# Performance work log

Hardware: AMD Instinct MI355X
Metric: run time of the kernel (lower is better)

The kernel has to match this reference:

```python
import jax, jax.numpy as jnp
import numpy as np
import math

D = 512; H = 8; DH = D // H; DFF = 4 * D
B = 128; S = 100; N_LAYERS = 6; VOCAB = 300 + 3
SCALE = 1.0 / math.sqrt(DH)


def _sinusoid(positions, d):
    # standard sinusoidal encoding, valid for negative (relative) positions too
    div = jnp.exp(jnp.arange(0, d, 2, dtype=jnp.float32) * (-math.log(10000.0) / d))
    ang = positions[:, None].astype(jnp.float32) * div[None, :]
    pe = jnp.zeros((positions.shape[0], d), dtype=jnp.float32)
    pe = pe.at[:, 0::2].set(jnp.sin(ang))
    pe = pe.at[:, 1::2].set(jnp.cos(ang))
    return pe


def _layernorm(x, g, b):
    m = jnp.mean(x, -1, keepdims=True)
    v = jnp.mean(jnp.square(x - m), -1, keepdims=True)
    return (x - m) * jax.lax.rsqrt(v + 1e-5) * g + b


def setup_inputs():
    key = jax.random.key(0)
    ks = jax.random.split(key, 16)
    s = 0.05
    n = lambda i, shape: jax.random.normal(ks[i], shape, dtype=jnp.float32) * s
    return {
        'input_ids': jax.random.randint(ks[0], (B, S), 0, VOCAB, dtype=jnp.int32),
        'src_len': jax.random.randint(ks[1], (B,), 1, S + 1, dtype=jnp.int32),
        'emb': n(2, (VOCAB, D)),
        'Wq': n(3, (D, D)), 'Wkv': n(4, (D, 2 * D)), 'Wpos': n(5, (D, D)), 'Wout': n(6, (D, D)),
        'u': n(7, (H, DH)), 'v': n(8, (H, DH)),
        'nmerge_g': jnp.ones((D,), jnp.float32), 'nmerge_b': jnp.zeros((D,), jnp.float32),
        'p1_w': n(9, (D, DFF)), 'p1_b': jnp.zeros((DFF,), jnp.float32),
        'p2_w': n(10, (DFF, D)), 'p2_b': jnp.zeros((D,), jnp.float32),
        'g1_w': n(11, (D, D)), 'g1_b': jnp.zeros((D,), jnp.float32),
        'g2_w': n(12, (D, D)), 'g2_b': jnp.full((D,), -3.0, jnp.float32),
    }


def _rel_attention(x, key_mask, Wq, Wkv, Wout, u, v, k_pos, rel_idx):
    # x: [B,S,D]; key_mask: [B,S] True = padded (masked out)
    q = (x @ Wq).reshape(B, S, H, DH)
    kv = (x @ Wkv).reshape(B, S, H, 2 * DH)
    k, vv = kv[..., :DH], kv[..., DH:]
    content = jnp.einsum('bqhd,bkhd->bhqk', q + u, k)
    pos = jnp.einsum('bqhd,rhd->bhqr', q + v, k_pos)               # r: 2S-1 relative offsets
    pos = jnp.take_along_axis(pos, rel_idx[None, None], axis=-1)   # [B,H,S,S] via rel-shift
    scores = (content + pos) * SCALE
    scores = jnp.where(key_mask[:, None, None, :], -1e9, scores)
    att = jax.nn.softmax(scores, axis=-1)
    out = jnp.einsum('bhqk,bkhd->bqhd', att, vv).reshape(B, S, D)
    return out @ Wout


def reference(input_ids, src_len, emb, Wq, Wkv, Wpos, Wout, u, v, nmerge_g, nmerge_b, p1_w, p1_b, p2_w, p2_b, g1_w, g1_b, g2_w, g2_b):
    # embedding + absolute sinusoidal positional encoding (scale=1.0)
    src = emb[input_ids] + _sinusoid(jnp.arange(S), D)[None]
    key_mask = jnp.arange(S)[None, :] >= src_len[:, None]          # True = masked
    # relative-position keys: offsets q-k ordered S-1 .. -(S-1)
    rel = jnp.arange(S - 1, -S, -1)
    k_pos = (_sinusoid(rel, D) @ Wpos).reshape(2 * S - 1, H, DH)
    i = jnp.arange(S)
    rel_idx = (S - 1) - i[:, None] + i[None, :]                    # (q,k) -> index of offset q-k
    for _ in range(N_LAYERS):  # universal transformer: one shared layer applied N times
        a = _rel_attention(src, key_mask, Wq, Wkv, Wout, u, v, k_pos, rel_idx)
        net = _layernorm(src + a, nmerge_g, nmerge_b)
        proj = jnp.tanh(jax.nn.relu(net @ p1_w + p1_b) @ p2_w + p2_b)
        bgate = jax.nn.sigmoid(jax.nn.relu(net @ g1_w + g1_b) @ g2_w + g2_b)
        src = src * (1.0 - bgate) + proj * bgate                   # NDR gated residual
    return src
```

## Files before the change

kernel.cpp:

```cpp
#include <hip/hip_runtime.h>
#include <hip/hip_bf16.h>
#include <math.h>

#define BB 128
#define SS 100
#define DD 512
#define HH 8
#define DHH 64
#define DFFF 2048
#define RR 199
#define MM (BB*SS)
#define NLAYERS 6
#define SCALE_ 0.125f

typedef __attribute__((ext_vector_type(8))) short bf16x8;
typedef __attribute__((ext_vector_type(4))) short bf16x4;
typedef __attribute__((ext_vector_type(4))) float floatx4;

__device__ inline unsigned short f2bf(float f) {
    union { float f; unsigned u; } c; c.f = f;
    unsigned r = c.u + 0x7FFFu + ((c.u >> 16) & 1u);
    return (unsigned short)(r >> 16);
}
__device__ inline float bf2f(unsigned short h) {
    union { unsigned u; float f; } c; c.u = ((unsigned)h) << 16;
    return c.f;
}
__device__ inline void split8(const float* x, bf16x8& hi, bf16x8& lo) {
    #pragma unroll
    for (int i = 0; i < 8; i++) {
        unsigned short h_ = f2bf(x[i]);
        hi[i] = (short)h_;
        lo[i] = (short)f2bf(x[i] - bf2f(h_));
    }
}
__device__ inline void gl2lds16(const unsigned short* g, unsigned short* l) {
    __builtin_amdgcn_global_load_lds(
        (const __attribute__((address_space(1))) void*)g,
        (__attribute__((address_space(3))) void*)l, 16, 0, 0);
}
__device__ inline bf16x8 ld8_u8align(const unsigned short* p) {
    bf16x4 a = *(const bf16x4*)p;
    bf16x4 b = *(const bf16x4*)(p + 4);
    return __builtin_shufflevector(a, b, 0, 1, 2, 3, 4, 5, 6, 7);
}

#define PANEL(buf, rows, r_, k_) ((buf) + ((size_t)((k_) >> 3) * (rows) + (r_)) * 8 + ((k_) & 7))

__global__ void embed_kernel(const int* __restrict__ ids, const float* __restrict__ emb,
                             float* __restrict__ src, unsigned short* __restrict__ srcbf) {
    int r  = blockIdx.x;
    int s  = r % SS;
    int id = ids[r];
    int d0 = threadIdx.x * 4;
    const float c = logf(10000.0f) / 512.0f;
    unsigned short pk[4];
    #pragma unroll
    for (int jj = 0; jj < 4; jj++) {
        int d  = d0 + jj;
        int j2 = d & ~1;
        float freq = expf(-(float)j2 * c);
        float ang  = (float)s * freq;
        float pe   = (d & 1) ? cosf(ang) : sinf(ang);
        float x = emb[id * DD + d] + pe;
        src[r * DD + d] = x;
        pk[jj] = f2bf(x);
    }
    *(uint2*)PANEL(srcbf, MM, r, d0) = *(uint2*)pk;
}

__global__ void kpos_kernel(const float* __restrict__ Wpos, unsigned short* __restrict__ kp) {
    int r = blockIdx.x;
    float p = (float)(SS - 1 - r);
    __shared__ float pe[DD];
    int t = threadIdx.x;
    const float c = logf(10000.0f) / 512.0f;
    {
        int j2 = t & ~1;
        float freq = expf(-(float)j2 * c);
        float ang  = p * freq;
        pe[t] = (t & 1) ? cosf(ang) : sinf(ang);
    }
    __syncthreads();
    float acc = 0.0f;
    for (int k = 0; k < DD; k++) acc += pe[k] * Wpos[k * DD + t];
    kp[r * DD + t] = f2bf(acc);
}

__global__ void wtr_kernel(const float* __restrict__ W, unsigned short* __restrict__ Wt,
                           int K, int N) {
    int idx = blockIdx.x * 256 + threadIdx.x;
    if (idx >= K * N) return;
    int k = idx / N, n = idx - k * N;
    *PANEL(Wt, N, n, k) = f2bf(W[idx]);
}

template<int ACT, int CMODE, int BN>
__global__ __launch_bounds__(256) void mgemm(const unsigned short* __restrict__ A,
                                             const unsigned short* __restrict__ Bt,
                                             const float* __restrict__ bias,
                                             float* __restrict__ Cf,
                                             unsigned short* __restrict__ Cb,
                                             int M, int N, int K,
                                             const float* __restrict__ Px) {
    const int NF = BN / 32;
    int nm = M >> 7, nn = N / BN;
    int bid = blockIdx.x;
    int xcd = bid & 7, slot = bid >> 3;
    int c0 = (xcd * nm) >> 3, c1 = ((xcd + 1) * nm) >> 3;
    int cm = c1 - c0;
    if (slot >= cm * nn) return;
    int m0 = (c0 + (slot % cm)) * 128;
    int n0 = (slot / cm) * BN;

    __shared__ __align__(16) unsigned short As[4 * 128 * 8];
    __shared__ __align__(16) unsigned short Bs[4 * BN * 8];
    int t = threadIdx.x, lane = t & 63, wave = t >> 6;
    int quad = lane >> 4, l16 = lane & 15;
    int wm = (wave & 1) * 64, wn = (wave >> 1) * (BN / 2);

    floatx4 acc[4][4];
    #pragma unroll
    for (int i = 0; i < 4; i++)
        #pragma unroll
        for (int j = 0; j < NF; j++) acc[i][j] = (floatx4){0.f, 0.f, 0.f, 0.f};

    for (int k0 = 0; k0 < K; k0 += 32) {
        __syncthreads();
        {
            const unsigned short* gA = A + ((size_t)((k0 >> 3) + wave) * M + m0) * 8;
            unsigned short* lA = As + wave * 128 * 8;
            gl2lds16(gA + lane * 8,        lA + lane * 8);
            gl2lds16(gA + (64 + lane) * 8, lA + (64 + lane) * 8);
        }
        {
            const unsigned short* gB = Bt + ((size_t)((k0 >> 3) + wave) * N + n0) * 8;
            unsigned short* lB = Bs + wave * BN * 8;
            gl2lds16(gB + lane * 8, lB + lane * 8);
            if (BN == 128) gl2lds16(gB + (64 + lane) * 8, lB + (64 + lane) * 8);
        }
        __syncthreads();
        bf16x8 af[4], bfv[4];
        #pragma unroll
        for (int mf = 0; mf < 4; mf++)
            af[mf] = *(const bf16x8*)(As + (quad * 128 + wm + mf * 16 + l16) * 8);
        #pragma unroll
        for (int nf = 0; nf < NF; nf++)
            bfv[nf] = *(const bf16x8*)(Bs + (quad * BN + wn + nf * 16 + l16) * 8);
        #pragma unroll
        for (int mf = 0; mf < 4; mf++)
            #pragma unroll
            for (int nf = 0; nf < NF; nf++)
                acc[mf][nf] = __builtin_amdgcn_mfma_f32_16x16x32_bf16(
                                  af[mf], bfv[nf], acc[mf][nf], 0, 0, 0);
    }

    #pragma unroll
    for (int nf = 0; nf < NF; nf++) {
        int col = n0 + wn + nf * 16 + l16;
        float bv = bias ? bias[col] : 0.0f;
        #pragma unroll
        for (int mf = 0; mf < 4; mf++) {
            #pragma unroll
            for (int r = 0; r < 4; r++) {
                int row = m0 + wm + mf * 16 + quad * 4 + r;
                float x = acc[mf][nf][r] + bv;
                if (ACT == 1) x = fmaxf(x, 0.0f);
                else if (ACT == 2) x = tanhf(x);
                if (CMODE == 0)      Cf[(size_t)row * N + col] = x;
                else if (CMODE == 1) *PANEL(Cb, M, row, col) = f2bf(x);
                else if (CMODE == 2) Cb[(size_t)row * N + col] = f2bf(x);
                else {
                    float xg = 1.0f / (1.0f + expf(-x));
                    size_t o = (size_t)row * N + col;
                    float out = Cf[o] * (1.0f - xg) + Px[o] * xg;
                    Cf[o] = out;
                    *PANEL(Cb, M, row, col) = f2bf(out);
                }
            }
        }
    }
}
static inline int mgemm_grid(int M, int N, int BN) {
    int nm = M >> 7, nn = N / BN;
    int cmmax = 0;
    for (int x = 0; x < 8; x++) {
        int c = ((x + 1) * nm) / 8 - (x * nm) / 8;
        if (c > cmmax) cmmax = c;
    }
    return 8 * cmmax * nn;
}

#define LKP 0
#define LK  12800
#define LV  19456
#define LPS 27648
#define PSW 116
__global__ __launch_bounds__(512, 4) void attn_kernel3(
        const float* __restrict__ q, const unsigned short* __restrict__ kvb,
        const unsigned short* __restrict__ kpbf, const float* __restrict__ u,
        const float* __restrict__ v, const int* __restrict__ len_,
        unsigned short* __restrict__ outp) {
    __shared__ __align__(16) unsigned short lds[40640];
    int b = blockIdx.x >> 3, h = blockIdx.x & 7;
    int t = threadIdx.x, wave = t >> 6, lane = t & 63;
    int quad = lane >> 4, l16 = lane & 15;

    {
        int r8 = lane >> 3;
        int cc = (lane & 7) ^ r8;
        for (int i = wave; i < 25; i += 8) {
            int row = i * 8 + r8;
            gl2lds16(kpbf + (size_t)row * DD + h * 64 + cc * 8,
                     lds + LKP + i * 512 + lane * 8);
        }
        for (int i = wave; i < 13; i += 8) {
            int row = i * 8 + r8;
            gl2lds16(kvb + (size_t)(b * SS + row) * 1024 + h * 128 + cc * 8,
                     lds + LK + i * 512 + lane * 8);
        }
    }
    for (int idx = t; idx < 8192; idx += 512) {
        int j = idx >> 6, d = idx & 63;
        unsigned short vv = kvb[(size_t)(b * SS + j) * 1024 + h * 128 + 64 + d];
        lds[LV + d * 128 + (((j >> 3) ^ (d & 15)) << 3) + (j & 7)] = vv;
    }
    int len = len_[b];
    float ua[2][8], va[2][8];
    #pragma unroll
    for (int kf = 0; kf < 2; kf++)
        #pragma unroll
        for (int i = 0; i < 8; i++) {
            ua[kf][i] = u[h * 64 + kf * 32 + quad * 8 + i];
            va[kf][i] = v[h * 64 + kf * 32 + quad * 8 + i];
        }
    __syncthreads();
    if (wave >= 7) return;

    int s = wave;
    unsigned short* psc = lds + LPS + wave * (16 * PSW);

    int iq = s * 16 + l16; if (iq > 99) iq = 99;
    const float* qrow = q + ((size_t)(b * SS + iq)) * DD + h * 64;
    bf16x8 qu_h[2], qu_l[2], qv_h[2], qv_l[2];
    #pragma unroll
    for (int kf = 0; kf < 2; kf++) {
        float4 q0 = *(const float4*)(qrow + kf * 32 + quad * 8);
        float4 q1 = *(const float4*)(qrow + kf * 32 + quad * 8 + 4);
        float qa[8] = {q0.x, q0.y, q0.z, q0.w, q1.x, q1.y, q1.z, q1.w};
        float xu[8], xv[8];
        #pragma unroll
        for (int i = 0; i < 8; i++) { xu[i] = qa[i] + ua[kf][i]; xv[i] = qa[i] + va[kf][i]; }
        split8(xu, qu_h[kf], qu_l[kf]);
        split8(xv, qv_h[kf], qv_l[kf]);
    }
    floatx4 cacc[7];
    #pragma unroll
    for (int nt = 0; nt < 7; nt++) cacc[nt] = (floatx4){0.f, 0.f, 0.f, 0.f};
    #pragma unroll
    for (int nt = 0; nt < 7; nt++) {
        int rr = nt * 16 + l16;
        #pragma unroll
        for (int kf = 0; kf < 2; kf++) {
            int ch = kf * 4 + quad;
            bf16x8 kb = *(const bf16x8*)(lds + LK + rr * 64 + ((ch ^ (rr & 7)) << 3));
            cacc[nt] = __builtin_amdgcn_mfma_f32_16x16x32_bf16(qu_h[kf], kb, cacc[nt], 0, 0, 0);
            cacc[nt] = __builtin_amdgcn_mfma_f32_16x16x32_bf16(qu_l[kf], kb, cacc[nt], 0, 0, 0);
        }
    }
    int w0 = 84 - 16 * s; if (w0 < 0) w0 = 0;
    {
        floatx4 pacc[8];
        #pragma unroll
        for (int nt = 0; nt < 8; nt++) pacc[nt] = (floatx4){0.f, 0.f, 0.f, 0.f};
        #pragma unroll
        for (int nt = 0; nt < 8; nt++) {
            int rr = w0 + nt * 16 + l16;
            #pragma unroll
            for (int kf = 0; kf < 2; kf++) {
                int ch = kf * 4 + quad;
                bf16x8 pb = *(const bf16x8*)(lds + LKP + rr * 64 + ((ch ^ (rr & 7)) << 3));
                pacc[nt] = __builtin_amdgcn_mfma_f32_16x16x32_bf16(qv_h[kf], pb, pacc[nt], 0, 0, 0);
                pacc[nt] = __builtin_amdgcn_mfma_f32_16x16x32_bf16(qv_l[kf], pb, pacc[nt], 0, 0, 0);
            }
        }
        #pragma unroll
        for (int nt = 0; nt < 7; nt++)
            #pragma unroll
            for (int r = 0; r < 4; r++)
                psc[(quad * 4 + r) * PSW + nt * 16 + l16] = f2bf(pacc[nt][r]);
        if (l16 < 4)
            #pragma unroll
            for (int r = 0; r < 4; r++)
                psc[(quad * 4 + r) * PSW + 112 + l16] = f2bf(pacc[7][r]);
    }
    float sc[7][4];
    #pragma unroll
    for (int nt = 0; nt < 7; nt++)
        #pragma unroll
        for (int r = 0; r < 4; r++) {
            int irow = s * 16 + quad * 4 + r;
            int j = nt * 16 + l16;
            int ro = 99 - irow + j - w0;
            ro = ro < 0 ? 0 : (ro > PSW - 1 ? PSW - 1 : ro);
            float val = (cacc[nt][r] + bf2f(psc[(quad * 4 + r) * PSW + ro])) * SCALE_;
            sc[nt][r] = (j < len) ? val : -1e9f;
        }
    float inv[4];
    #pragma unroll
    for (int r = 0; r < 4; r++) {
        float m_ = sc[0][r];
        #pragma unroll
        for (int nt = 1; nt < 7; nt++) m_ = fmaxf(m_, sc[nt][r]);
        #pragma unroll
        for (int o = 8; o; o >>= 1) m_ = fmaxf(m_, __shfl_xor(m_, o));
        float s_ = 0.f;
        #pragma unroll
        for (int nt = 0; nt < 7; nt++) { sc[nt][r] = expf(sc[nt][r] - m_); s_ += sc[nt][r]; }
        #pragma unroll
        for (int o = 8; o; o >>= 1) s_ += __shfl_xor(s_, o);
        inv[r] = 1.0f / s_;
    }
    bf16x8 zero8 = (bf16x8){0, 0, 0, 0, 0, 0, 0, 0};
    floatx4 oacc[4];
    #pragma unroll
    for (int ntd = 0; ntd < 4; ntd++) oacc[ntd] = (floatx4){0.f, 0.f, 0.f, 0.f};
    #pragma unroll
    for (int pass = 0; pass < 2; pass++) {
        #pragma unroll
        for (int r = 0; r < 4; r++) {
            int row = quad * 4 + r;
            #pragma unroll
            for (int nt = 0; nt < 7; nt++) {
                float pv = sc[nt][r] * inv[r];
                unsigned short ph = f2bf(pv);
                psc[row * PSW + nt * 16 + l16] =
                    (pass == 0) ? ph : f2bf(pv - bf2f(ph));
            }
        }
        bf16x8 pa[4];
        #pragma unroll
        for (int kf = 0; kf < 3; kf++)
            pa[kf] = ld8_u8align(psc + l16 * PSW + kf * 32 + quad * 8);
        pa[3] = (quad < 2) ? ld8_u8align(psc + l16 * PSW + 96 + quad * 8) : zero8;
        #pragma unroll
        for (int ntd = 0; ntd < 4; ntd++) {
            int d = ntd * 16 + l16;
            #pragma unroll
            for (int kf = 0; kf < 4; kf++) {
                int ch = kf * 4 + quad;
                bf16x8 bv = *(const bf16x8*)(lds + LV + d * 128 + ((ch ^ (d & 15)) << 3));
                oacc[ntd] = __builtin_amdgcn_mfma_f32_16x16x32_bf16(pa[kf], bv, oacc[ntd], 0, 0, 0);
            }
        }
    }
    #pragma unroll
    for (int ntd = 0; ntd < 4; ntd++)
        #pragma unroll
        for (int r = 0; r < 4; r++) {
            int irow = s * 16 + quad * 4 + r;
            if (irow < 100) {
                int col = h * 64 + ntd * 16 + l16;
                int row = b * SS + irow;
                *PANEL(outp, MM, row, col) = f2bf(oacc[ntd][r]);
            }
        }
}

__global__ void ln_kernel(const float* __restrict__ x, const float* __restrict__ a,
                          const float* __restrict__ g, const float* __restrict__ bb,
                          unsigned short* __restrict__ outp) {
    int r = blockIdx.x;
    int t = threadIdx.x;
    float4 xv = *(const float4*)(x + (size_t)r * DD + t * 4);
    float4 av = *(const float4*)(a + (size_t)r * DD + t * 4);
    float v0 = xv.x + av.x, v1 = xv.y + av.y, v2 = xv.z + av.z, v3 = xv.w + av.w;
    float sum = v0 + v1 + v2 + v3;
    float sq  = v0 * v0 + v1 * v1 + v2 * v2 + v3 * v3;
    #pragma unroll
    for (int o = 32; o > 0; o >>= 1) {
        sum += __shfl_down(sum, o);
        sq  += __shfl_down(sq, o);
    }
    __shared__ float ls[2], lq[2];
    if ((t & 63) == 0) { ls[t >> 6] = sum; lq[t >> 6] = sq; }
    __syncthreads();
    float S_ = ls[0] + ls[1], Q_ = lq[0] + lq[1];
    float m   = S_ / 512.0f;
    float var = Q_ / 512.0f - m * m;
    float rs  = rsqrtf(var + 1e-5f);
    float4 gv = *(const float4*)(g  + t * 4);
    float4 bv = *(const float4*)(bb + t * 4);
    unsigned short pk[4];
    pk[0] = f2bf((v0 - m) * rs * gv.x + bv.x);
    pk[1] = f2bf((v1 - m) * rs * gv.y + bv.y);
    pk[2] = f2bf((v2 - m) * rs * gv.z + bv.z);
    pk[3] = f2bf((v3 - m) * rs * gv.w + bv.w);
    *(uint2*)PANEL(outp, MM, r, t * 4) = *(uint2*)pk;
}

extern "C" void kernel_launch(void* const* d_in, const int* in_sizes, int n_in,
                              void* d_out, int out_size, void* d_ws, size_t ws_size,
                              hipStream_t stream) {
    const int*   ids     = (const int*)  d_in[0];
    const int*   src_len = (const int*)  d_in[1];
    const float* emb     = (const float*)d_in[2];
    const float* Wq      = (const float*)d_in[3];
    const float* Wkv     = (const float*)d_in[4];
    const float* Wpos    = (const float*)d_in[5];
    const float* Wout    = (const float*)d_in[6];
    const float* u       = (const float*)d_in[7];
    const float* v       = (const float*)d_in[8];
    const float* ng      = (const float*)d_in[9];
    const float* nb      = (const float*)d_in[10];
    const float* p1_w    = (const float*)d_in[11];
    const float* p1_b    = (const float*)d_in[12];
    const float* p2_w    = (const float*)d_in[13];
    const float* p2_b    = (const float*)d_in[14];
    const float* g1_w    = (const float*)d_in[15];
    const float* g1_b    = (const float*)d_in[16];
    const float* g2_w    = (const float*)d_in[17];
    const float* g2_b    = (const float*)d_in[18];

    float* src = (float*)d_out;

    float* ws     = (float*)d_ws;
    float* q      = ws;
    float* t1     = q    + (size_t)MM * DD;
    float* proj   = t1   + (size_t)MM * DD;
    float* bg     = proj + (size_t)MM * DD;
    unsigned short* kpbf  = (unsigned short*)(bg + (size_t)MM * DD);
    unsigned short* srcbf = kpbf  + (size_t)RR * DD;
    unsigned short* netbf = srcbf + (size_t)MM * DD;
    unsigned short* t0p   = netbf + (size_t)MM * DD;
    unsigned short* kvb   = t0p   + (size_t)MM * DD;
    unsigned short* ffb   = kvb   + (size_t)MM * 2 * DD;
    unsigned short* hgb   = ffb   + (size_t)MM * DFFF;
    unsigned short* wq_t   = hgb   + (size_t)MM * DD;
    unsigned short* wkv_t  = wq_t   + 512 * 512;
    unsigned short* wout_t = wkv_t  + 1024 * 512;
    unsigned short* p1_t   = wout_t + 512 * 512;
    unsigned short* p2_t   = p1_t   + 2048 * 512;
    unsigned short* g1_t   = p2_t   + 512 * 2048;
    unsigned short* g2_t   = g1_t   + 512 * 512;

    embed_kernel<<<MM, 128, 0, stream>>>(ids, emb, src, srcbf);
    kpos_kernel<<<RR, DD, 0, stream>>>(Wpos, kpbf);
    wtr_kernel<<<(512*512 +255)/256, 256, 0, stream>>>(Wq,   wq_t,   512, 512);
    wtr_kernel<<<(512*1024+255)/256, 256, 0, stream>>>(Wkv,  wkv_t,  512, 1024);
    wtr_kernel<<<(512*512 +255)/256, 256, 0, stream>>>(Wout, wout_t, 512, 512);
    wtr_kernel<<<(512*2048+255)/256, 256, 0, stream>>>(p1_w, p1_t,   512, 2048);
    wtr_kernel<<<(2048*512+255)/256, 256, 0, stream>>>(p2_w, p2_t,   2048, 512);
    wtr_kernel<<<(512*512 +255)/256, 256, 0, stream>>>(g1_w, g1_t,   512, 512);
    wtr_kernel<<<(512*512 +255)/256, 256, 0, stream>>>(g2_w, g2_t,   512, 512);

    int g64   = mgemm_grid(MM, 512, 64);
    int g128k = mgemm_grid(MM, 1024, 128);
    int g128f = mgemm_grid(MM, 2048, 128);

    for (int layer = 0; layer < NLAYERS; layer++) {
        mgemm<0,0,64><<<g64, 256, 0, stream>>>(
            srcbf, wq_t, (const float*)nullptr, q, (unsigned short*)nullptr,
            MM, 512, 512, (const float*)nullptr);
        mgemm<0,2,128><<<g128k, 256, 0, stream>>>(
            srcbf, wkv_t, (const float*)nullptr, (float*)nullptr, kvb,
            MM, 1024, 512, (const float*)nullptr);
        attn_kernel3<<<BB * HH, 512, 0, stream>>>(q, kvb, kpbf, u, v, src_len, t0p);
        mgemm<0,0,64><<<g64, 256, 0, stream>>>(
            t0p, wout_t, (const float*)nullptr, t1, (unsigned short*)nullptr,
            MM, 512, 512, (const float*)nullptr);
        ln_kernel<<<MM, 128, 0, stream>>>(src, t1, ng, nb, netbf);
        mgemm<1,1,128><<<g128f, 256, 0, stream>>>(
            netbf, p1_t, p1_b, (float*)nullptr, ffb, MM, 2048, 512,
            (const float*)nullptr);
        mgemm<2,0,64><<<g64, 256, 0, stream>>>(
            ffb, p2_t, p2_b, proj, (unsigned short*)nullptr, MM, 512, 2048,
            (const float*)nullptr);
        mgemm<1,1,64><<<g64, 256, 0, stream>>>(
            netbf, g1_t, g1_b, (float*)nullptr, hgb, MM, 512, 512,
            (const float*)nullptr);
        mgemm<0,3,64><<<g64, 256, 0, stream>>>(
            hgb, g2_t, g2_b, src, srcbf, MM, 512, 512, proj);
    }
}
```

Before: 2.021 ms.

## Fuse QKV and P1/G1 GEMMs, double-buffer LDS staging, coalesce bf16 epilogue stores

Concatenates Wq and Wkv into one transposed weight so Q, K and V come from a single GEMM launch, and likewise concatenates p1_w and g1_w (with their biases) so the FFN and gate first layers share one launch over netbf. The GEMM main loop now double-buffers its LDS tiles, issuing the next k-slice load before computing the current one, which removes one barrier per iteration. Bf16 outputs are staged through shared memory and written as 16-byte vector stores instead of scattered 2-byte stores. In exchange the kernel uses more shared memory (which may lower occupancy) and has more complex epilogue branching.

```diff
diff --git a/kernel.cpp b/kernel.cpp
--- a/kernel.cpp
+++ b/kernel.cpp
@@ -87,12 +87,26 @@
     kp[r * DD + t] = f2bf(acc);
 }
 
-__global__ void wtr_kernel(const float* __restrict__ W, unsigned short* __restrict__ Wt,
-                           int K, int N) {
+__global__ void wtr_off_kernel(const float* __restrict__ W, unsigned short* __restrict__ Wt,
+                               int K, int Nsrc, int Ntot, int n_off) {
     int idx = blockIdx.x * 256 + threadIdx.x;
-    if (idx >= K * N) return;
-    int k = idx / N, n = idx - k * N;
-    *PANEL(Wt, N, n, k) = f2bf(W[idx]);
+    if (idx >= K * Nsrc) return;
+    int k = idx / Nsrc, n = idx - k * Nsrc;
+    *PANEL(Wt, Ntot, n_off + n, k) = f2bf(W[idx]);
+}
+
+template<int BN>
+__device__ __forceinline__ void stage_tile(const unsigned short* A, const unsigned short* Bt,
+        unsigned short* smem, int it, int buf, int m0, int n0, int M, int N,
+        int wave, int lane) {
+    const unsigned short* gA = A + ((size_t)(it * 4 + wave) * M + m0) * 8;
+    unsigned short* lA = smem + buf * 4096 + wave * 1024;
+    gl2lds16(gA + lane * 8,        lA + lane * 8);
+    gl2lds16(gA + (64 + lane) * 8, lA + (64 + lane) * 8);
+    const unsigned short* gB = Bt + ((size_t)(it * 4 + wave) * N + n0) * 8;
+    unsigned short* lB = smem + 8192 + buf * (BN * 32) + wave * (BN * 8);
+    gl2lds16(gB + lane * 8, lB + lane * 8);
+    if (BN == 128) gl2lds16(gB + (64 + lane) * 8, lB + (64 + lane) * 8);
 }
 
 template<int ACT, int CMODE, int BN>
@@ -101,9 +115,14 @@
                                              const float* __restrict__ bias,
                                              float* __restrict__ Cf,
                                              unsigned short* __restrict__ Cb,
+                                             unsigned short* __restrict__ Cb2,
                                              int M, int N, int K,
                                              const float* __restrict__ Px) {
-    const int NF = BN / 32;
+    const int NF  = BN / 32;
+    const int STG = 8192 + 2 * BN * 32;
+    const int SCR = 128 * (BN + 8);
+    __shared__ __align__(16) unsigned short smem[(STG > SCR) ? STG : SCR];
+
     int nm = M >> 7, nn = N / BN;
     int bid = blockIdx.x;
     int xcd = bid & 7, slot = bid >> 3;
@@ -113,8 +132,6 @@
     int m0 = (c0 + (slot % cm)) * 128;
     int n0 = (slot / cm) * BN;
 
-    __shared__ __align__(16) unsigned short As[4 * 128 * 8];
-    __shared__ __align__(16) unsigned short Bs[4 * BN * 8];
     int t = threadIdx.x, lane = t & 63, wave = t >> 6;
     int quad = lane >> 4, l16 = lane & 15;
     int wm = (wave & 1) * 64, wn = (wave >> 1) * (BN / 2);
@@ -125,21 +142,14 @@
         #pragma unroll
         for (int j = 0; j < NF; j++) acc[i][j] = (floatx4){0.f, 0.f, 0.f, 0.f};
 
-    for (int k0 = 0; k0 < K; k0 += 32) {
+    int nit = K >> 5;
+    stage_tile<BN>(A, Bt, smem, 0, 0, m0, n0, M, N, wave, lane);
+    for (int it = 0; it < nit; it++) {
         __syncthreads();
-        {
-            const unsigned short* gA = A + ((size_t)((k0 >> 3) + wave) * M + m0) * 8;
-            unsigned short* lA = As + wave * 128 * 8;
-            gl2lds16(gA + lane * 8,        lA + lane * 8);
-            gl2lds16(gA + (64 + lane) * 8, lA + (64 + lane) * 8);
-        }
-        {
-            const unsigned short* gB = Bt + ((size_t)((k0 >> 3) + wave) * N + n0) * 8;
-            unsigned short* lB = Bs + wave * BN * 8;
-            gl2lds16(gB + lane * 8, lB + lane * 8);
-            if (BN == 128) gl2lds16(gB + (64 + lane) * 8, lB + (64 + lane) * 8);
-        }
-        __syncthreads();
+        if (it + 1 < nit)
+            stage_tile<BN>(A, Bt, smem, it + 1, (it + 1) & 1, m0, n0, M, N, wave, lane);
+        const unsigned short* As = smem + (it & 1) * 4096;
+        const unsigned short* Bs = smem + 8192 + (it & 1) * (BN * 32);
         bf16x8 af[4], bfv[4];
         #pragma unroll
         for (int mf = 0; mf < 4; mf++)
@@ -154,29 +164,85 @@
                 acc[mf][nf] = __builtin_amdgcn_mfma_f32_16x16x32_bf16(
                                   af[mf], bfv[nf], acc[mf][nf], 0, 0, 0);
     }
-
-    #pragma unroll
-    for (int nf = 0; nf < NF; nf++) {
-        int col = n0 + wn + nf * 16 + l16;
-        float bv = bias ? bias[col] : 0.0f;
-        #pragma unroll
-        for (int mf = 0; mf < 4; mf++) {
-            #pragma unroll
-            for (int r = 0; r < 4; r++) {
-                int row = m0 + wm + mf * 16 + quad * 4 + r;
-                float x = acc[mf][nf][r] + bv;
-                if (ACT == 1) x = fmaxf(x, 0.0f);
-                else if (ACT == 2) x = tanhf(x);
-                if (CMODE == 0)      Cf[(size_t)row * N + col] = x;
-                else if (CMODE == 1) *PANEL(Cb, M, row, col) = f2bf(x);
-                else if (CMODE == 2) Cb[(size_t)row * N + col] = f2bf(x);
-                else {
+    __syncthreads();
+
+    const int ST = BN + 8;
+    if (CMODE == 0 || (CMODE == 4 && n0 < 512)) {
+        int ldc = (CMODE == 4) ? 512 : N;
+        #pragma unroll
+        for (int nf = 0; nf < NF; nf++) {
+            int col = n0 + wn + nf * 16 + l16;
+            float bv = bias ? bias[col] : 0.0f;
+            #pragma unroll
+            for (int mf = 0; mf < 4; mf++)
+                #pragma unroll
+                for (int r = 0; r < 4; r++) {
+                    int row = m0 + wm + mf * 16 + quad * 4 + r;
+                    float x = acc[mf][nf][r] + bv;
+                    if (ACT == 1) x = fmaxf(x, 0.f);
+                    else if (ACT == 2) x = tanhf(x);
+                    Cf[(size_t)row * ldc + col] = x;
+                }
+        }
+    } else if (CMODE == 3) {
+        #pragma unroll
+        for (int nf = 0; nf < NF; nf++) {
+            int col = n0 + wn + nf * 16 + l16;
+            float bv = bias ? bias[col] : 0.0f;
+            #pragma unroll
+            for (int mf = 0; mf < 4; mf++)
+                #pragma unroll
+                for (int r = 0; r < 4; r++) {
+                    int rrow = wm + mf * 16 + quad * 4 + r;
+                    float x = acc[mf][nf][r] + bv;
                     float xg = 1.0f / (1.0f + expf(-x));
-                    size_t o = (size_t)row * N + col;
+                    size_t o = (size_t)(m0 + rrow) * N + col;
                     float out = Cf[o] * (1.0f - xg) + Px[o] * xg;
                     Cf[o] = out;
-                    *PANEL(Cb, M, row, col) = f2bf(out);
+                    smem[rrow * ST + wn + nf * 16 + l16] = f2bf(out);
                 }
+        }
+        __syncthreads();
+        int row = t & 127, hb = t >> 7;
+        for (int i = hb; i < BN / 8; i += 2) {
+            uint4 vd = *(const uint4*)(smem + row * ST + i * 8);
+            int gcol = n0 + i * 8;
+            *(uint4*)(Cb + ((size_t)(gcol >> 3) * M + m0 + row) * 8) = vd;
+        }
+    } else {
+        #pragma unroll
+        for (int nf = 0; nf < NF; nf++) {
+            int col = n0 + wn + nf * 16 + l16;
+            float bv = bias ? bias[col] : 0.0f;
+            #pragma unroll
+            for (int mf = 0; mf < 4; mf++)
+                #pragma unroll
+                for (int r = 0; r < 4; r++) {
+                    int rrow = wm + mf * 16 + quad * 4 + r;
+                    float x = acc[mf][nf][r] + bv;
+                    if (ACT == 1) x = fmaxf(x, 0.f);
+                    else if (ACT == 2) x = tanhf(x);
+                    smem[rrow * ST + wn + nf * 16 + l16] = f2bf(x);
+                }
+        }
+        __syncthreads();
+        if (CMODE == 4) {
+            int rr0 = t >> 4, chk = t & 15;
+            for (int rr = rr0; rr < 128; rr += 16) {
+                uint4 vd = *(const uint4*)(smem + rr * ST + chk * 8);
+                *(uint4*)(Cb + (size_t)(m0 + rr) * 1024 + (n0 - 512) + chk * 8) = vd;
+            }
+        } else {
+            int row = t & 127, hb = t >> 7;
+            for (int i = hb; i < BN / 8; i += 2) {
+                uint4 vd = *(const uint4*)(smem + row * ST + i * 8);
+                int gcol = n0 + i * 8;
+                unsigned short* dst;
+                if (CMODE == 5 && gcol >= 2048)
+                    dst = Cb2 + ((size_t)((gcol - 2048) >> 3) * M + m0 + row) * 8;
+                else
+                    dst = Cb + ((size_t)(gcol >> 3) * M + m0 + row) * 8;
+                *(uint4*)dst = vd;
             }
         }
     }
@@ -428,58 +494,53 @@
     float* q      = ws;
     float* t1     = q    + (size_t)MM * DD;
     float* proj   = t1   + (size_t)MM * DD;
-    float* bg     = proj + (size_t)MM * DD;
-    unsigned short* kpbf  = (unsigned short*)(bg + (size_t)MM * DD);
+    float* p1g1_b = proj + (size_t)MM * DD;
+    unsigned short* kpbf  = (unsigned short*)(p1g1_b + 4096);
     unsigned short* srcbf = kpbf  + (size_t)RR * DD;
     unsigned short* netbf = srcbf + (size_t)MM * DD;
     unsigned short* t0p   = netbf + (size_t)MM * DD;
     unsigned short* kvb   = t0p   + (size_t)MM * DD;
     unsigned short* ffb   = kvb   + (size_t)MM * 2 * DD;
     unsigned short* hgb   = ffb   + (size_t)MM * DFFF;
-    unsigned short* wq_t   = hgb   + (size_t)MM * DD;
-    unsigned short* wkv_t  = wq_t   + 512 * 512;
-    unsigned short* wout_t = wkv_t  + 1024 * 512;
-    unsigned short* p1_t   = wout_t + 512 * 512;
-    unsigned short* p2_t   = p1_t   + 2048 * 512;
-    unsigned short* g1_t   = p2_t   + 512 * 2048;
-    unsigned short* g2_t   = g1_t   + 512 * 512;
+    unsigned short* qkv_t  = hgb   + (size_t)MM * DD;
+    unsigned short* wout_t = qkv_t  + 1536 * 512;
+    unsigned short* p1g1_t = wout_t + 512 * 512;
+    unsigned short* p2_t   = p1g1_t + 2560 * 512;
+    unsigned short* g2_t   = p2_t   + 512 * 2048;
 
     embed_kernel<<<MM, 128, 0, stream>>>(ids, emb, src, srcbf);
     kpos_kernel<<<RR, DD, 0, stream>>>(Wpos, kpbf);
-    wtr_kernel<<<(512*512 +255)/256, 256, 0, stream>>>(Wq,   wq_t,   512, 512);
-    wtr_kernel<<<(512*1024+255)/256, 256, 0, stream>>>(Wkv,  wkv_t,  512, 1024);
-    wtr_kernel<<<(512*512 +255)/256, 256, 0, stream>>>(Wout, wout_t, 512, 512);
-    wtr_kernel<<<(512*2048+255)/256, 256, 0, stream>>>(p1_w, p1_t,   512, 2048);
-    wtr_kernel<<<(2048*512+255)/256, 256, 0, stream>>>(p2_w, p2_t,   2048, 512);
-    wtr_kernel<<<(512*512 +255)/256, 256, 0, stream>>>(g1_w, g1_t,   512, 512);
-    wtr_kernel<<<(512*512 +255)/256, 256, 0, stream>>>(g2_w, g2_t,   512, 512);
-
-    int g64   = mgemm_grid(MM, 512, 64);
-    int g128k = mgemm_grid(MM, 1024, 128);
-    int g128f = mgemm_grid(MM, 2048, 128);
+    wtr_off_kernel<<<(512*512 +255)/256, 256, 0, stream>>>(Wq,   qkv_t,  512, 512,  1536, 0);
+    wtr_off_kernel<<<(512*1024+255)/256, 256, 0, stream>>>(Wkv,  qkv_t,  512, 1024, 1536, 512);
+    wtr_off_kernel<<<(512*512 +255)/256, 256, 0, stream>>>(Wout, wout_t, 512, 512,  512,  0);
+    wtr_off_kernel<<<(512*2048+255)/256, 256, 0, stream>>>(p1_w, p1g1_t, 512, 2048, 2560, 0);
+    wtr_off_kernel<<<(512*512 +255)/256, 256, 0, stream>>>(g1_w, p1g1_t, 512, 512,  2560, 2048);
+    wtr_off_kernel<<<(2048*512+255)/256, 256, 0, stream>>>(p2_w, p2_t,   2048, 512, 512,  0);
+    wtr_off_kernel<<<(512*512 +255)/256, 256, 0, stream>>>(g2_w, g2_t,   512, 512,  512,  0);
+    hipMemcpyAsync(p1g1_b,        p1_b, 2048 * sizeof(float), hipMemcpyDeviceToDevice, stream);
+    hipMemcpyAsync(p1g1_b + 2048, g1_b,  512 * sizeof(float), hipMemcpyDeviceToDevice, stream);
+
+    int gqkv = mgemm_grid(MM, 1536, 128);
+    int g64  = mgemm_grid(MM, 512, 64);
+    int gp1  = mgemm_grid(MM, 2560, 128);
 
     for (int layer = 0; layer < NLAYERS; layer++) {
-        mgemm<0,0,64><<<g64, 256, 0, stream>>>(
-            srcbf, wq_t, (const float*)nullptr, q, (unsigned short*)nullptr,
-            MM, 512, 512, (const float*)nullptr);
-        mgemm<0,2,128><<<g128k, 256, 0, stream>>>(
-            srcbf, wkv_t, (const float*)nullptr, (float*)nullptr, kvb,
-            MM, 1024, 512, (const float*)nullptr);
+        mgemm<0,4,128><<<gqkv, 256, 0, stream>>>(
+            srcbf, qkv_t, (const float*)nullptr, q, kvb, (unsigned short*)nullptr,
+            MM, 1536, 512, (const float*)nullptr);
         attn_kernel3<<<BB * HH, 512, 0, stream>>>(q, kvb, kpbf, u, v, src_len, t0p);
         mgemm<0,0,64><<<g64, 256, 0, stream>>>(
             t0p, wout_t, (const float*)nullptr, t1, (unsigned short*)nullptr,
-            MM, 512, 512, (const float*)nullptr);
+            (unsigned short*)nullptr, MM, 512, 512, (const float*)nullptr);
         ln_kernel<<<MM, 128, 0, stream>>>(src, t1, ng, nb, netbf);
-        mgemm<1,1,128><<<g128f, 256, 0, stream>>>(
-            netbf, p1_t, p1_b, (float*)nullptr, ffb, MM, 2048, 512,
-            (const float*)nullptr);
+        mgemm<1,5,128><<<gp1, 256, 0, stream>>>(
+            netbf, p1g1_t, p1g1_b, (float*)nullptr, ffb, hgb,
+            MM, 2560, 512, (const float*)nullptr);
         mgemm<2,0,64><<<g64, 256, 0, stream>>>(
-            ffb, p2_t, p2_b, proj, (unsigned short*)nullptr, MM, 512, 2048,
-            (const float*)nullptr);
-        mgemm<1,1,64><<<g64, 256, 0, stream>>>(
-            netbf, g1_t, g1_b, (float*)nullptr, hgb, MM, 512, 512,
-            (const float*)nullptr);
+            ffb, p2_t, p2_b, proj, (unsigned short*)nullptr, (unsigned short*)nullptr,
+            MM, 512, 2048, (const float*)nullptr);
         mgemm<0,3,64><<<g64, 256, 0, stream>>>(
-            hgb, g2_t, g2_b, src, srcbf, MM, 512, 512, proj);
-    }
-}
+            hgb, g2_t, g2_b, src, srcbf, (unsigned short*)nullptr,
+            MM, 512, 512, proj);
+    }
+}
```

After: 1.671 ms. -17.4%, faster.
